# Optimization experiments

Hardware: AMD Instinct MI355X
Metric: run time of the kernel (lower is better)

Reference implementation:

```python
import jax, jax.numpy as jnp
import numpy as np


def setup_inputs() -> dict:
    key = jax.random.key(0)
    k1, k2, k3, k4 = jax.random.split(key, 4)
    B, T, S, D = 32, 512, 1024, 1024
    inp = jax.random.normal(k1, (B, T, D), dtype=jnp.float32)
    ctx = jax.random.normal(k2, (B, S, D), dtype=jnp.float32)
    W_in = jax.random.normal(k3, (D, D), dtype=jnp.float32) * (1.0 / np.sqrt(D))
    W_out = jax.random.normal(k4, (D, 2 * D), dtype=jnp.float32) * (1.0 / np.sqrt(2 * D))
    return {"input": inp, "context": ctx, "W_in": W_in, "W_out": W_out}


def reference(input, context, W_in, W_out):
    # GlobalAttention, attn_type='general', no mask, no coverage, tgt_len > 1.
    B, T, D = input.shape
    S = context.shape[1]
    # score: (W_in h_t) . h_s   -> [B, T, S]
    h_t = jnp.einsum('btd,ed->bte', input, W_in)           # linear_in (no bias)
    align = jnp.einsum('btd,bsd->bts', h_t, context)
    align_vectors = jax.nn.softmax(align, axis=-1)          # [B, T, S]
    # weighted sum of context
    c = jnp.einsum('bts,bsd->btd', align_vectors, context)  # [B, T, D]
    # concat [c, input] -> linear_out (no bias for 'general') -> tanh
    concat_c = jnp.concatenate([c, input], axis=-1)          # [B, T, 2D]
    attn_h = jnp.tanh(jnp.einsum('btf,df->btd', concat_c, W_out))
    # not one_step: transpose to [T, B, ...]
    attn_h = jnp.transpose(attn_h, (1, 0, 2))
    align_vectors = jnp.transpose(align_vectors, (1, 0, 2))
    return attn_h, align_vectors
```

## Files before the change

### kernel.cpp

```cpp
#include <hip/hip_runtime.h>
#include <hip/hip_bf16.h>


typedef short bf16x8 __attribute__((ext_vector_type(8)));
typedef float f32x4 __attribute__((ext_vector_type(4)));
typedef unsigned short us;

#define NB 32
#define NT_ 512
#define NS 1024
#define ND 1024

__device__ inline us f2bf(float x) {
  unsigned u = __float_as_uint(x);
  u += 0x7FFFu + ((u >> 16) & 1u);
  return (us)(u >> 16);
}
__device__ inline float bf2f(us h) { return __uint_as_float(((unsigned)h) << 16); }

__device__ inline void store_split(us* __restrict__ hi, us* __restrict__ lo, size_t idx, float v) {
  us h = f2bf(v);
  hi[idx] = h;
  lo[idx] = f2bf(v - bf2f(h));
}

__global__ void ga_split(const float* __restrict__ src, us* __restrict__ hi,
                         us* __restrict__ lo, long n) {
  long i0 = ((long)blockIdx.x * blockDim.x + threadIdx.x) * 4;
  long stride = (long)gridDim.x * blockDim.x * 4;
  for (long i = i0; i < n; i += stride) {
    float4 v = *reinterpret_cast<const float4*>(src + i);
    ushort4 h, l;
    h.x = f2bf(v.x); l.x = f2bf(v.x - bf2f(h.x));
    h.y = f2bf(v.y); l.y = f2bf(v.y - bf2f(h.y));
    h.z = f2bf(v.z); l.z = f2bf(v.z - bf2f(h.z));
    h.w = f2bf(v.w); l.w = f2bf(v.w - bf2f(h.w));
    *reinterpret_cast<ushort4*>(hi + i) = h;
    *reinterpret_cast<ushort4*>(lo + i) = l;
  }
}

__global__ void ga_cvt(const float* __restrict__ src, us* __restrict__ dst, long n) {
  long i0 = ((long)blockIdx.x * blockDim.x + threadIdx.x) * 4;
  long stride = (long)gridDim.x * blockDim.x * 4;
  for (long i = i0; i < n; i += stride) {
    float4 v = *reinterpret_cast<const float4*>(src + i);
    ushort4 h;
    h.x = f2bf(v.x); h.y = f2bf(v.y); h.z = f2bf(v.z); h.w = f2bf(v.w);
    *reinterpret_cast<ushort4*>(dst + i) = h;
  }
}

__global__ void ga_transpose_split(const float* __restrict__ ctx, us* __restrict__ tHi,
                                   us* __restrict__ tLo) {
  __shared__ float tile[64][65];
  int s0 = blockIdx.x << 6, d0 = blockIdx.y << 6, b = blockIdx.z;
  const float* src = ctx + (size_t)b * NS * ND;
  int tid = threadIdx.x;
#pragma unroll
  for (int i = 0; i < 16; ++i) {
    int lin = (i << 8) + tid;
    int r = lin >> 6, c = lin & 63;
    tile[r][c] = src[(size_t)(s0 + r) * ND + d0 + c];
  }
  __syncthreads();
  us* oH = tHi + (size_t)b * ND * NS;
  us* oL = tLo + (size_t)b * ND * NS;
#pragma unroll
  for (int i = 0; i < 16; ++i) {
    int lin = (i << 8) + tid;
    int dr = lin >> 6, sc = lin & 63;
    float v = tile[sc][dr];
    size_t o = (size_t)(d0 + dr) * NS + s0 + sc;
    us h = f2bf(v);
    oH[o] = h;
    oL[o] = f2bf(v - bf2f(h));
  }
}

__global__ __launch_bounds__(256) void ga_softmax(float* __restrict__ al,
                                                  us* __restrict__ pHi, us* __restrict__ pLo) {
  int row = blockIdx.x;
  int tid = threadIdx.x;
  float* p = al + (size_t)row * NS;
  float4 v = *reinterpret_cast<const float4*>(p + (tid << 2));
  float m = fmaxf(fmaxf(v.x, v.y), fmaxf(v.z, v.w));
#pragma unroll
  for (int off = 32; off; off >>= 1) m = fmaxf(m, __shfl_xor(m, off));
  __shared__ float rmax[4], rsum[4];
  int wv = tid >> 6, ln = tid & 63;
  if (ln == 0) rmax[wv] = m;
  __syncthreads();
  m = fmaxf(fmaxf(rmax[0], rmax[1]), fmaxf(rmax[2], rmax[3]));
  float4 e;
  e.x = __expf(v.x - m); e.y = __expf(v.y - m);
  e.z = __expf(v.z - m); e.w = __expf(v.w - m);
  float s = e.x + e.y + e.z + e.w;
#pragma unroll
  for (int off = 32; off; off >>= 1) s += __shfl_xor(s, off);
  if (ln == 0) rsum[wv] = s;
  __syncthreads();
  s = rsum[0] + rsum[1] + rsum[2] + rsum[3];
  float inv = 1.0f / s;
  e.x *= inv; e.y *= inv; e.z *= inv; e.w *= inv;
  *reinterpret_cast<float4*>(p + (tid << 2)) = e;
  int t = row >> 5, b = row & 31;
  size_t o = ((size_t)b * NT_ + t) * NS + (tid << 2);
  ushort4 h, l;
  h.x = f2bf(e.x); l.x = f2bf(e.x - bf2f(h.x));
  h.y = f2bf(e.y); l.y = f2bf(e.y - bf2f(h.y));
  h.z = f2bf(e.z); l.z = f2bf(e.z - bf2f(h.z));
  h.w = f2bf(e.w); l.w = f2bf(e.w - bf2f(h.w));
  *reinterpret_cast<ushort4*>(pHi + o) = h;
  *reinterpret_cast<ushort4*>(pLo + o) = l;
}

__device__ inline void gload16(const us* g, void* l) {
  __builtin_amdgcn_global_load_lds((const __attribute__((address_space(1))) unsigned int*)g,
                                   (__attribute__((address_space(3))) unsigned int*)l, 16, 0, 0);
}

__device__ inline f32x4 mfma16(bf16x8 a, bf16x8 b, f32x4 c) {
  return __builtin_amdgcn_mfma_f32_16x16x32_bf16(a, b, c, 0, 0, 0);
}

#define VM0 asm volatile("s_waitcnt vmcnt(0)" ::: "memory")
#define VMS do { if constexpr (MODE != 3)                                          \
                   asm volatile("s_waitcnt vmcnt(8)" ::: "memory");                \
                 else asm volatile("s_waitcnt vmcnt(6)" ::: "memory"); } while (0)

#define STG_AH(C) do {                                                             \
    const us* b_; long col_;                                                       \
    if constexpr (MODE == 3) {                                                     \
      if ((C) < 32) { b_ = pA0; col_ = (long)(C) << 5; }                           \
      else          { b_ = pA2; col_ = (long)((C) - 32) << 5; }                    \
    } else { b_ = pA0; col_ = (long)(C) << 5; }                                    \
    const us* g_ = b_ + col_ + aOff;                                               \
    char* d_ = lb + (((C) & 1) ? BUFSZ : 0) + (tid << 4);                          \
    gload16(g_, d_); gload16(g_ + 131072, d_ + 8192);                              \
  } while (0)

#define STG_AL(C) do {                                                             \
    const us* b_; long col_;                                                       \
    if constexpr (MODE == 3) {                                                     \
      if ((C) < 32) { b_ = pA1; col_ = (long)(C) << 5; }                           \
      else          { b_ = pA3; col_ = (long)((C) - 32) << 5; }                    \
    } else { b_ = pA1; col_ = (long)(C) << 5; }                                    \
    const us* g_ = b_ + col_ + aOff;                                               \
    char* d_ = lb + (((C) & 1) ? BUFSZ : 0) + 16384 + (tid << 4);                  \
    gload16(g_, d_); gload16(g_ + 131072, d_ + 8192);                              \
  } while (0)

#define STG_BH(C) do {                                                             \
    const us* g_ = pB0 + ((long)(C) << 5) + bOff;                                  \
    char* d_ = lb + (((C) & 1) ? BUFSZ : 0) + 32768 + (tid << 4);                  \
    gload16(g_, d_); gload16(g_ + ((long)LDB << 7), d_ + 8192);                    \
  } while (0)

#define STG_BL(C) do {                                                             \
    const us* g_ = pB1 + ((long)(C) << 5) + bOff;                                  \
    char* d_ = lb + (((C) & 1) ? BUFSZ : 0) + 49152 + (tid << 4);                  \
    gload16(g_, d_); gload16(g_ + ((long)LDB << 7), d_ + 8192);                    \
  } while (0)

#define RD_A8(BP, PO) do {                                                         \
    const char* p_ = (BP) + (PO) + aRd;                                            \
    _Pragma("unroll") for (int m_ = 0; m_ < 8; ++m_)                               \
      a8[m_] = *(const bf16x8*)(p_ + (m_ << 10) + colx);                           \
  } while (0)

#define RD_B4(BP, PO, ARR) do {                                                    \
    const char* p_ = (BP) + (PO) + bRd;                                            \
    _Pragma("unroll") for (int n_ = 0; n_ < 4; ++n_)                               \
      ARR[n_] = *(const bf16x8*)(p_ + (n_ << 10) + colx);                          \
  } while (0)

#define MM32(BB)                                                                   \
  _Pragma("unroll") for (int m_ = 0; m_ < 8; ++m_)                                 \
  _Pragma("unroll") for (int n_ = 0; n_ < 4; ++n_)                                 \
    acc[m_][n_] = mfma16(a8[m_], BB[n_], acc[m_][n_])

#define PH(RDS, MMQ, POST) do {                                                    \
    __builtin_amdgcn_s_barrier();                                                  \
    RDS;                                                                           \
    __builtin_amdgcn_s_setprio(1);                                                 \
    MMQ;                                                                           \
    __builtin_amdgcn_s_setprio(0);                                                 \
    POST;                                                                          \
  } while (0)

template <int MODE>
__global__ __launch_bounds__(512, 1) void ga_gc(
    const us* __restrict__ Ahi, const us* __restrict__ Alo,
    const us* __restrict__ A2hi, const us* __restrict__ A2lo,
    const us* __restrict__ Bhi, const us* __restrict__ Blo,
    void* __restrict__ out0, void* __restrict__ out1,
    long astride, long bstride) {
  constexpr int LDB = (MODE == 3) ? 2048 : 1024;
  constexpr int NC = (MODE == 3) ? 64 : 32;
  constexpr int BUFSZ = (MODE == 3) ? 49152 : 65536;
  __shared__ __align__(16) char lds[2 * BUFSZ];
  char* lb = lds;
  const int tid = threadIdx.x;
  const int lane = tid & 63;
  const int fr = lane & 15;
  const int wv = tid >> 6;
  const int wr = wv >> 2, wc = wv & 3;

  int rowA, colB, bz;
  if constexpr (MODE == 1 || MODE == 2) {
    const int bi = blockIdx.x;
    const int j = bi >> 3;
    bz = ((bi & 7) << 2) + (j & 3);
    const int panel = j >> 2;
    rowA = (panel & 1) << 8;
    colB = (panel >> 1) << 8;
  } else {
    rowA = blockIdx.x << 8;
    colB = blockIdx.y << 8;
    bz = blockIdx.z;
  }

  const us* pA0 = Ahi + (size_t)bz * astride + (size_t)rowA * 1024;
  const us* pA1 = Alo + (size_t)bz * astride + (size_t)rowA * 1024;
  const us* pA2 = (MODE == 3) ? A2hi + (size_t)rowA * 1024 : nullptr;
  const us* pA3 = (MODE == 3) ? A2lo + (size_t)rowA * 1024 : nullptr;
  const us* pB0 = Bhi + (size_t)bz * bstride + (size_t)colB * LDB;
  const us* pB1 = (MODE == 3) ? nullptr : Blo + (size_t)bz * bstride + (size_t)colB * LDB;

  const int swc = ((tid & 3) ^ ((tid >> 3) & 3)) << 3;
  const long aOff = (long)(tid >> 2) * 1024 + swc;
  const long bOff = (long)(tid >> 2) * LDB + swc;

  const int colx = (((lane >> 4) ^ ((fr >> 1) & 3)) << 4);
  const int aRd = (wr << 13) + (fr << 6);
  const int bRd = (wc << 12) + (fr << 6);

  bf16x8 a8[8], bh[4], bl2[4];
  f32x4 zero = {0.f, 0.f, 0.f, 0.f};
  f32x4 acc[8][4];
#pragma unroll
  for (int i = 0; i < 8; ++i)
#pragma unroll
    for (int k = 0; k < 4; ++k) acc[i][k] = zero;

  if constexpr (MODE != 3) {
    STG_AH(0); STG_BH(0); STG_BL(0); STG_AL(0);
    STG_AH(1); STG_BH(1); STG_BL(1);
  } else {
    STG_AH(0); STG_BH(0); STG_AL(0);
    STG_AH(1); STG_BH(1);
  }
  VM0;
  __builtin_amdgcn_s_barrier();

  if constexpr (MODE != 3) {
    for (int c = 0; c < NC - 2; ++c) {
      const char* bp = lb + ((c & 1) ? BUFSZ : 0);
      PH({ RD_B4(bp, 32768, bh); RD_A8(bp, 0); }, MM32(bh),
         { STG_AL(c + 1); VMS; });
      PH({ RD_B4(bp, 49152, bl2); }, MM32(bl2),
         { STG_AH(c + 2); STG_BH(c + 2); VMS; });
      PH({ RD_A8(bp, 16384); }, MM32(bh),
         { STG_BL(c + 2); VMS; });
    }
    {
      const char* bp = lb + (((NC - 2) & 1) ? BUFSZ : 0);
      PH({ RD_B4(bp, 32768, bh); RD_A8(bp, 0); }, MM32(bh),
         { STG_AL(NC - 1); VM0; });
      PH({ RD_B4(bp, 49152, bl2); }, MM32(bl2), {});
      PH({ RD_A8(bp, 16384); }, MM32(bh), {});
    }
    {
      const char* bp = lb + (((NC - 1) & 1) ? BUFSZ : 0);
      PH({ RD_B4(bp, 32768, bh); RD_A8(bp, 0); }, MM32(bh), {});
      PH({ RD_B4(bp, 49152, bl2); }, MM32(bl2), {});
      PH({ RD_A8(bp, 16384); }, MM32(bh), {});
    }
  } else {
    for (int c = 0; c < NC - 2; ++c) {
      const char* bp = lb + ((c & 1) ? BUFSZ : 0);
      PH({ RD_B4(bp, 32768, bh); RD_A8(bp, 0); }, MM32(bh),
         { STG_AL(c + 1); VMS; });
      PH({ RD_A8(bp, 16384); }, MM32(bh),
         { STG_AH(c + 2); STG_BH(c + 2); VMS; });
    }
    {
      const char* bp = lb + (((NC - 2) & 1) ? BUFSZ : 0);
      PH({ RD_B4(bp, 32768, bh); RD_A8(bp, 0); }, MM32(bh),
         { STG_AL(NC - 1); VM0; });
      PH({ RD_A8(bp, 16384); }, MM32(bh), {});
    }
    {
      const char* bp = lb + (((NC - 1) & 1) ? BUFSZ : 0);
      PH({ RD_B4(bp, 32768, bh); RD_A8(bp, 0); }, MM32(bh), {});
      PH({ RD_A8(bp, 16384); }, MM32(bh), {});
    }
  }

#pragma unroll
  for (int mf = 0; mf < 8; ++mf)
#pragma unroll
    for (int nf = 0; nf < 4; ++nf)
#pragma unroll
      for (int j = 0; j < 4; ++j) {
        int r = rowA + (wr << 7) + (mf << 4) + (((lane >> 4) & 3) << 2) + j;
        int c = colB + (wc << 6) + (nf << 4) + fr;
        float v = acc[mf][nf][j];
        if constexpr (MODE == 0) {
          store_split((us*)out0, (us*)out1, (size_t)r * 1024 + c, v);
        } else if constexpr (MODE == 1) {
          ((float*)out0)[((size_t)r * NB + bz) * NS + c] = v;
        } else if constexpr (MODE == 2) {
          store_split((us*)out0, (us*)out1, ((size_t)bz * 512 + r) * 1024 + c, v);
        } else {
          int bb = r >> 9, tt2 = r & 511;
          ((float*)out0)[((size_t)tt2 * NB + bb) * ND + c] = tanhf(v);
        }
      }
}

extern "C" void kernel_launch(void* const* d_in, const int* in_sizes, int n_in,
                              void* d_out, int out_size, void* d_ws, size_t ws_size,
                              hipStream_t stream) {
  (void)in_sizes; (void)n_in; (void)out_size; (void)ws_size;
  const float* inp = (const float*)d_in[0];
  const float* ctx = (const float*)d_in[1];
  const float* Win = (const float*)d_in[2];
  const float* Wout = (const float*)d_in[3];
  float* out = (float*)d_out;

  char* w = (char*)d_ws;
  us* ctx_hi  = (us*)(w + 0);
  us* c_hi    = (us*)(w + 0);
  us* c_lo    = (us*)(w + 33554432);
  us* ctx_lo  = (us*)(w + 67108864);
  us* p_hi    = (us*)(w + 67108864);
  us* p_lo    = (us*)(w + 100663296);
  us* in_hi   = (us*)(w + 134217728);
  us* in_lo   = (us*)(w + 167772160);
  us* h_hi    = (us*)(w + 201326592);
  us* h_lo    = (us*)(w + 234881024);
  us* ctxT_lo = (us*)(w + 201326592);
  us* win_hi  = (us*)(w + 268435456);
  us* win_lo  = (us*)(w + 270532608);
  us* wout_b  = (us*)(w + 272629760);

  us* ctxT_hi = (us*)d_out;
  float* alignOut = out + 16777216;

  ga_split<<<2048, 256, 0, stream>>>(inp, in_hi, in_lo, 16777216L);
  ga_split<<<2048, 256, 0, stream>>>(ctx, ctx_hi, ctx_lo, 33554432L);
  ga_split<<<512, 256, 0, stream>>>(Win, win_hi, win_lo, 1048576L);
  ga_cvt<<<512, 256, 0, stream>>>(Wout, wout_b, 2097152L);

  ga_gc<0><<<dim3(64, 4, 1), 512, 0, stream>>>(in_hi, in_lo, nullptr, nullptr,
                                               win_hi, win_lo, h_hi, h_lo, 0L, 0L);
  ga_gc<1><<<dim3(256, 1, 1), 512, 0, stream>>>(h_hi, h_lo, nullptr, nullptr,
                                                ctx_hi, ctx_lo, alignOut, nullptr,
                                                524288L, 1048576L);
  ga_transpose_split<<<dim3(16, 16, 32), 256, 0, stream>>>(ctx, ctxT_hi, ctxT_lo);
  ga_softmax<<<16384, 256, 0, stream>>>(alignOut, p_hi, p_lo);
  ga_gc<2><<<dim3(256, 1, 1), 512, 0, stream>>>(p_hi, p_lo, nullptr, nullptr,
                                                ctxT_hi, ctxT_lo, c_hi, c_lo,
                                                524288L, 1048576L);
  ga_gc<3><<<dim3(64, 4, 1), 512, 0, stream>>>(c_hi, c_lo, in_hi, in_lo,
                                               wout_b, nullptr, out, nullptr, 0L, 0L);
}
```

Measured before the change: 555.4 us.

## Shrink GEMM tiles to 128x128 with 256-thread blocks, two per CU

Switches the split-bf16 GEMM kernel from 256x256 tiles on 512-thread blocks (one per CU) to 128x128 tiles on 256-thread blocks with launch bounds allowing two blocks per CU. LDS buffers, staging offsets, wave layout, fragment reads and the phase schedule are all rebuilt. The lo-part products are now merged into two phases per k-chunk instead of three, with new vmcnt waits. The goal is more blocks and better latency hiding across CUs, at the cost of lower arithmetic intensity per tile and more global and L2 traffic.

```diff
diff --git a/kernel.cpp b/kernel.cpp
--- a/kernel.cpp
+++ b/kernel.cpp
@@ -125,9 +125,8 @@
 }
 
 #define VM0 asm volatile("s_waitcnt vmcnt(0)" ::: "memory")
-#define VMS do { if constexpr (MODE != 3)                                          \
-                   asm volatile("s_waitcnt vmcnt(8)" ::: "memory");                \
-                 else asm volatile("s_waitcnt vmcnt(6)" ::: "memory"); } while (0)
+#define VM2 asm volatile("s_waitcnt vmcnt(2)" ::: "memory")
+#define VM4 asm volatile("s_waitcnt vmcnt(4)" ::: "memory")
 
 #define STG_AH(C) do {                                                             \
     const us* b_; long col_;                                                       \
@@ -137,7 +136,7 @@
     } else { b_ = pA0; col_ = (long)(C) << 5; }                                    \
     const us* g_ = b_ + col_ + aOff;                                               \
     char* d_ = lb + (((C) & 1) ? BUFSZ : 0) + (tid << 4);                          \
-    gload16(g_, d_); gload16(g_ + 131072, d_ + 8192);                              \
+    gload16(g_, d_); gload16(g_ + 65536, d_ + 4096);                               \
   } while (0)
 
 #define STG_AL(C) do {                                                             \
@@ -147,38 +146,32 @@
       else          { b_ = pA3; col_ = (long)((C) - 32) << 5; }                    \
     } else { b_ = pA1; col_ = (long)(C) << 5; }                                    \
     const us* g_ = b_ + col_ + aOff;                                               \
-    char* d_ = lb + (((C) & 1) ? BUFSZ : 0) + 16384 + (tid << 4);                  \
-    gload16(g_, d_); gload16(g_ + 131072, d_ + 8192);                              \
+    char* d_ = lb + (((C) & 1) ? BUFSZ : 0) + 8192 + (tid << 4);                   \
+    gload16(g_, d_); gload16(g_ + 65536, d_ + 4096);                               \
   } while (0)
 
 #define STG_BH(C) do {                                                             \
     const us* g_ = pB0 + ((long)(C) << 5) + bOff;                                  \
-    char* d_ = lb + (((C) & 1) ? BUFSZ : 0) + 32768 + (tid << 4);                  \
-    gload16(g_, d_); gload16(g_ + ((long)LDB << 7), d_ + 8192);                    \
+    char* d_ = lb + (((C) & 1) ? BUFSZ : 0) + 16384 + (tid << 4);                  \
+    gload16(g_, d_); gload16(g_ + ((long)LDB << 6), d_ + 4096);                    \
   } while (0)
 
 #define STG_BL(C) do {                                                             \
     const us* g_ = pB1 + ((long)(C) << 5) + bOff;                                  \
-    char* d_ = lb + (((C) & 1) ? BUFSZ : 0) + 49152 + (tid << 4);                  \
-    gload16(g_, d_); gload16(g_ + ((long)LDB << 7), d_ + 8192);                    \
-  } while (0)
-
-#define RD_A8(BP, PO) do {                                                         \
-    const char* p_ = (BP) + (PO) + aRd;                                            \
-    _Pragma("unroll") for (int m_ = 0; m_ < 8; ++m_)                               \
-      a8[m_] = *(const bf16x8*)(p_ + (m_ << 10) + colx);                           \
-  } while (0)
-
-#define RD_B4(BP, PO, ARR) do {                                                    \
-    const char* p_ = (BP) + (PO) + bRd;                                            \
-    _Pragma("unroll") for (int n_ = 0; n_ < 4; ++n_)                               \
-      ARR[n_] = *(const bf16x8*)(p_ + (n_ << 10) + colx);                          \
-  } while (0)
-
-#define MM32(BB)                                                                   \
-  _Pragma("unroll") for (int m_ = 0; m_ < 8; ++m_)                                 \
+    char* d_ = lb + (((C) & 1) ? BUFSZ : 0) + 24576 + (tid << 4);                  \
+    gload16(g_, d_); gload16(g_ + ((long)LDB << 6), d_ + 4096);                    \
+  } while (0)
+
+#define RD4(BP, PO, BASE, ARR) do {                                                \
+    const char* p_ = (BP) + (PO) + (BASE);                                         \
+    _Pragma("unroll") for (int q_ = 0; q_ < 4; ++q_)                               \
+      ARR[q_] = *(const bf16x8*)(p_ + (q_ << 10) + colx);                          \
+  } while (0)
+
+#define MM16(AA, BB)                                                               \
+  _Pragma("unroll") for (int m_ = 0; m_ < 4; ++m_)                                 \
   _Pragma("unroll") for (int n_ = 0; n_ < 4; ++n_)                                 \
-    acc[m_][n_] = mfma16(a8[m_], BB[n_], acc[m_][n_])
+    acc[m_][n_] = mfma16(AA[m_], BB[n_], acc[m_][n_])
 
 #define PH(RDS, MMQ, POST) do {                                                    \
     __builtin_amdgcn_s_barrier();                                                  \
@@ -190,7 +183,7 @@
   } while (0)
 
 template <int MODE>
-__global__ __launch_bounds__(512, 1) void ga_gc(
+__global__ __launch_bounds__(256, 2) void ga_ge(
     const us* __restrict__ Ahi, const us* __restrict__ Alo,
     const us* __restrict__ A2hi, const us* __restrict__ A2lo,
     const us* __restrict__ Bhi, const us* __restrict__ Blo,
@@ -198,14 +191,14 @@
     long astride, long bstride) {
   constexpr int LDB = (MODE == 3) ? 2048 : 1024;
   constexpr int NC = (MODE == 3) ? 64 : 32;
-  constexpr int BUFSZ = (MODE == 3) ? 49152 : 65536;
+  constexpr int BUFSZ = (MODE == 3) ? 24576 : 32768;
   __shared__ __align__(16) char lds[2 * BUFSZ];
   char* lb = lds;
   const int tid = threadIdx.x;
   const int lane = tid & 63;
   const int fr = lane & 15;
   const int wv = tid >> 6;
-  const int wr = wv >> 2, wc = wv & 3;
+  const int wr = wv >> 1, wc = wv & 1;
 
   int rowA, colB, bz;
   if constexpr (MODE == 1 || MODE == 2) {
@@ -213,11 +206,11 @@
     const int j = bi >> 3;
     bz = ((bi & 7) << 2) + (j & 3);
     const int panel = j >> 2;
-    rowA = (panel & 1) << 8;
-    colB = (panel >> 1) << 8;
+    rowA = (panel & 3) << 7;
+    colB = (panel >> 2) << 7;
   } else {
-    rowA = blockIdx.x << 8;
-    colB = blockIdx.y << 8;
+    rowA = blockIdx.x << 7;
+    colB = blockIdx.y << 7;
     bz = blockIdx.z;
   }
 
@@ -233,20 +226,20 @@
   const long bOff = (long)(tid >> 2) * LDB + swc;
 
   const int colx = (((lane >> 4) ^ ((fr >> 1) & 3)) << 4);
-  const int aRd = (wr << 13) + (fr << 6);
+  const int aRd = (wr << 12) + (fr << 6);
   const int bRd = (wc << 12) + (fr << 6);
 
-  bf16x8 a8[8], bh[4], bl2[4];
+  bf16x8 ah[4], al[4], bh[4], bl[4];
   f32x4 zero = {0.f, 0.f, 0.f, 0.f};
-  f32x4 acc[8][4];
-#pragma unroll
-  for (int i = 0; i < 8; ++i)
+  f32x4 acc[4][4];
+#pragma unroll
+  for (int i = 0; i < 4; ++i)
 #pragma unroll
     for (int k = 0; k < 4; ++k) acc[i][k] = zero;
 
   if constexpr (MODE != 3) {
     STG_AH(0); STG_BH(0); STG_BL(0); STG_AL(0);
-    STG_AH(1); STG_BH(1); STG_BL(1);
+    STG_AH(1); STG_BH(1);
   } else {
     STG_AH(0); STG_BH(0); STG_AL(0);
     STG_AH(1); STG_BH(1);
@@ -257,54 +250,53 @@
   if constexpr (MODE != 3) {
     for (int c = 0; c < NC - 2; ++c) {
       const char* bp = lb + ((c & 1) ? BUFSZ : 0);
-      PH({ RD_B4(bp, 32768, bh); RD_A8(bp, 0); }, MM32(bh),
-         { STG_AL(c + 1); VMS; });
-      PH({ RD_B4(bp, 49152, bl2); }, MM32(bl2),
-         { STG_AH(c + 2); STG_BH(c + 2); VMS; });
-      PH({ RD_A8(bp, 16384); }, MM32(bh),
-         { STG_BL(c + 2); VMS; });
+      PH({ RD4(bp, 16384, bRd, bh); RD4(bp, 0, aRd, ah); }, MM16(ah, bh),
+         { STG_AL(c + 1); STG_BL(c + 1); VM4; });
+      PH({ RD4(bp, 24576, bRd, bl); RD4(bp, 8192, aRd, al); },
+         { MM16(ah, bl); MM16(al, bh); },
+         { STG_AH(c + 2); STG_BH(c + 2); VM4; });
     }
     {
       const char* bp = lb + (((NC - 2) & 1) ? BUFSZ : 0);
-      PH({ RD_B4(bp, 32768, bh); RD_A8(bp, 0); }, MM32(bh),
-         { STG_AL(NC - 1); VM0; });
-      PH({ RD_B4(bp, 49152, bl2); }, MM32(bl2), {});
-      PH({ RD_A8(bp, 16384); }, MM32(bh), {});
+      PH({ RD4(bp, 16384, bRd, bh); RD4(bp, 0, aRd, ah); }, MM16(ah, bh),
+         { STG_AL(NC - 1); STG_BL(NC - 1); VM0; });
+      PH({ RD4(bp, 24576, bRd, bl); RD4(bp, 8192, aRd, al); },
+         { MM16(ah, bl); MM16(al, bh); }, {});
     }
     {
       const char* bp = lb + (((NC - 1) & 1) ? BUFSZ : 0);
-      PH({ RD_B4(bp, 32768, bh); RD_A8(bp, 0); }, MM32(bh), {});
-      PH({ RD_B4(bp, 49152, bl2); }, MM32(bl2), {});
-      PH({ RD_A8(bp, 16384); }, MM32(bh), {});
+      PH({ RD4(bp, 16384, bRd, bh); RD4(bp, 0, aRd, ah); }, MM16(ah, bh), {});
+      PH({ RD4(bp, 24576, bRd, bl); RD4(bp, 8192, aRd, al); },
+         { MM16(ah, bl); MM16(al, bh); }, {});
     }
   } else {
     for (int c = 0; c < NC - 2; ++c) {
       const char* bp = lb + ((c & 1) ? BUFSZ : 0);
-      PH({ RD_B4(bp, 32768, bh); RD_A8(bp, 0); }, MM32(bh),
-         { STG_AL(c + 1); VMS; });
-      PH({ RD_A8(bp, 16384); }, MM32(bh),
-         { STG_AH(c + 2); STG_BH(c + 2); VMS; });
+      PH({ RD4(bp, 16384, bRd, bh); RD4(bp, 0, aRd, ah); }, MM16(ah, bh),
+         { STG_AL(c + 1); VM2; });
+      PH({ RD4(bp, 8192, aRd, al); }, MM16(al, bh),
+         { STG_AH(c + 2); STG_BH(c + 2); VM4; });
     }
     {
       const char* bp = lb + (((NC - 2) & 1) ? BUFSZ : 0);
-      PH({ RD_B4(bp, 32768, bh); RD_A8(bp, 0); }, MM32(bh),
+      PH({ RD4(bp, 16384, bRd, bh); RD4(bp, 0, aRd, ah); }, MM16(ah, bh),
          { STG_AL(NC - 1); VM0; });
-      PH({ RD_A8(bp, 16384); }, MM32(bh), {});
+      PH({ RD4(bp, 8192, aRd, al); }, MM16(al, bh), {});
     }
     {
       const char* bp = lb + (((NC - 1) & 1) ? BUFSZ : 0);
-      PH({ RD_B4(bp, 32768, bh); RD_A8(bp, 0); }, MM32(bh), {});
-      PH({ RD_A8(bp, 16384); }, MM32(bh), {});
-    }
-  }
-
-#pragma unroll
-  for (int mf = 0; mf < 8; ++mf)
+      PH({ RD4(bp, 16384, bRd, bh); RD4(bp, 0, aRd, ah); }, MM16(ah, bh), {});
+      PH({ RD4(bp, 8192, aRd, al); }, MM16(al, bh), {});
+    }
+  }
+
+#pragma unroll
+  for (int mf = 0; mf < 4; ++mf)
 #pragma unroll
     for (int nf = 0; nf < 4; ++nf)
 #pragma unroll
       for (int j = 0; j < 4; ++j) {
-        int r = rowA + (wr << 7) + (mf << 4) + (((lane >> 4) & 3) << 2) + j;
+        int r = rowA + (wr << 6) + (mf << 4) + (((lane >> 4) & 3) << 2) + j;
         int c = colB + (wc << 6) + (nf << 4) + fr;
         float v = acc[mf][nf][j];
         if constexpr (MODE == 0) {
@@ -354,16 +346,16 @@
   ga_split<<<512, 256, 0, stream>>>(Win, win_hi, win_lo, 1048576L);
   ga_cvt<<<512, 256, 0, stream>>>(Wout, wout_b, 2097152L);
 
-  ga_gc<0><<<dim3(64, 4, 1), 512, 0, stream>>>(in_hi, in_lo, nullptr, nullptr,
-                                               win_hi, win_lo, h_hi, h_lo, 0L, 0L);
-  ga_gc<1><<<dim3(256, 1, 1), 512, 0, stream>>>(h_hi, h_lo, nullptr, nullptr,
-                                                ctx_hi, ctx_lo, alignOut, nullptr,
-                                                524288L, 1048576L);
+  ga_ge<0><<<dim3(128, 8, 1), 256, 0, stream>>>(in_hi, in_lo, nullptr, nullptr,
+                                                win_hi, win_lo, h_hi, h_lo, 0L, 0L);
+  ga_ge<1><<<dim3(1024, 1, 1), 256, 0, stream>>>(h_hi, h_lo, nullptr, nullptr,
+                                                 ctx_hi, ctx_lo, alignOut, nullptr,
+                                                 524288L, 1048576L);
   ga_transpose_split<<<dim3(16, 16, 32), 256, 0, stream>>>(ctx, ctxT_hi, ctxT_lo);
   ga_softmax<<<16384, 256, 0, stream>>>(alignOut, p_hi, p_lo);
-  ga_gc<2><<<dim3(256, 1, 1), 512, 0, stream>>>(p_hi, p_lo, nullptr, nullptr,
-                                                ctxT_hi, ctxT_lo, c_hi, c_lo,
-                                                524288L, 1048576L);
-  ga_gc<3><<<dim3(64, 4, 1), 512, 0, stream>>>(c_hi, c_lo, in_hi, in_lo,
-                                               wout_b, nullptr, out, nullptr, 0L, 0L);
-}
+  ga_ge<2><<<dim3(1024, 1, 1), 256, 0, stream>>>(p_hi, p_lo, nullptr, nullptr,
+                                                 ctxT_hi, ctxT_lo, c_hi, c_lo,
+                                                 524288L, 1048576L);
+  ga_ge<3><<<dim3(128, 8, 1), 256, 0, stream>>>(c_hi, c_lo, in_hi, in_lo,
+                                                wout_b, nullptr, out, nullptr, 0L, 0L);
+}
```

After: 685.4 us. 23.4% more time.
